# Kernel optimization log

Hardware: AMD Instinct MI355X
Metric: run time of the kernel (lower is better)

The kernel has to match this reference:

```python
import jax, jax.numpy as jnp
import numpy as np

K_CLASSES = 5   # num support classes (5-way)
N_SHOT = 5      # supports per class


def setup_inputs() -> dict:
    key = jax.random.key(0)
    k0, k1, k2, k3 = jax.random.split(key, 4)
    b, bs, c, h, w = 32, K_CLASSES * N_SHOT, 512, 14, 14
    dk, dv = 128, 128
    return {
        "support_features": jax.random.normal(k0, (bs, c, h, w), jnp.float32),
        "query_features": jax.random.normal(k1, (b, c, h, w), jnp.float32),
        "support_labels": jnp.repeat(jnp.arange(K_CLASSES), N_SHOT).astype(jnp.int32),
        "W_qk": jax.random.normal(k2, (dk, c), jnp.float32) * 0.02,  # 1x1 conv weight
        "W_v": jax.random.normal(k3, (dv, c), jnp.float32) * 0.02,   # 1x1 conv weight
    }


def reference(support_features, query_features, support_labels, W_qk, W_v):
    scale = 1.0  # 1/temperature, temperature=1.0
    # 1x1 convs == channel-mixing einsums
    query_q = jnp.einsum('bchw,dc->bdhw', query_features, W_qk)
    query_v = jnp.einsum('bchw,dc->bdhw', query_features, W_v)
    supp_k = jnp.einsum('nchw,dc->ndhw', support_features, W_qk)
    supp_v = jnpveinsum = jnp.einsum('nchw,dc->ndhw', support_features, W_v)
    supp_v = jnpveinsum
    b, cv, h, w = query_v.shape

    # similarity over all supports: [b,h,w,n,i,j] (contracts dim_key)
    sim = jnp.einsum('bchw,ncij->bhwnij', query_q, supp_k) * scale

    # per-class masked softmax over the (n,i,j) axes restricted to that class's
    # supports == index_select + softmax in the original loop (labels balanced).
    cls_mask = support_labels[None, :] == jnp.arange(K_CLASSES)[:, None]  # [K,n]
    neg = jnp.finfo(sim.dtype).min
    sim_k = jnp.where(cls_mask[:, None, None, None, :, None, None], sim[None], neg)  # [K,b,h,w,n,i,j]
    attn = jax.nn.softmax(sim_k.reshape(K_CLASSES, b, h, w, -1), axis=-1)
    attn = attn.reshape(sim_k.shape)  # masked-out entries -> exactly 0

    # weighted sum of support values: [K,b,c,h,w]
    out = jnp.einsum('kbhwnij,ncij->kbchw', attn, supp_v)
    prototypes = jnp.transpose(out, (1, 0, 2, 3, 4)).reshape(b, K_CLASSES, -1)  # b k (c h w)
    query_v_flat = query_v.reshape(b, 1, -1)  # b () (c h w)
    return prototypes, query_v_flat
```

## Files before the change

kernel.cpp:

```cpp
#include <hip/hip_runtime.h>
#include <cstdint>
#include <cstddef>

#define NB   32
#define NSUP 25
#define KCLS 5
#define NC   512
#define ND   128
#define NP   196
#define JS   208
#define NIMG 57
#define SHIFT 8.0f

typedef __attribute__((ext_vector_type(8))) short short8;
typedef __attribute__((ext_vector_type(4))) float floatx4;

__device__ inline short f2bf(float x) {
  union { float f; uint32_t u; } v; v.f = x;
  uint32_t r = (v.u + 0x7FFFu + ((v.u >> 16) & 1u)) >> 16;
  return (short)(r & 0xFFFFu);
}
__device__ inline uint32_t pk2(float a, float b) {
  return (uint32_t)(uint16_t)f2bf(a) | ((uint32_t)(uint16_t)f2bf(b) << 16);
}

__global__ __launch_bounds__(256) void wconv_kernel(
    const float* __restrict__ Wqk, const float* __restrict__ Wv,
    uint16_t* __restrict__ Whi)
{
  const int f = (blockIdx.x * 256 + (int)threadIdx.x) * 8;
  const float* src = (f < ND * NC) ? (Wqk + f) : (Wv + f - ND * NC);
  short8 hv;
  #pragma unroll
  for (int i = 0; i < 8; ++i) hv[i] = f2bf(src[i]);
  *(short8*)(Whi + f) = hv;
}

__global__ __launch_bounds__(256) void gemm_kernel(
    const float* __restrict__ supp, const float* __restrict__ qry,
    const uint16_t* __restrict__ Whi,
    uint16_t* __restrict__ Qt, uint16_t* __restrict__ Kt,
    uint16_t* __restrict__ Vt, float* __restrict__ outVq)
{
  __shared__ float xs[NC * 17];
  const int bx = blockIdx.x;
  const int t16 = bx % 13, img = bx / 13;
  const int tid = (int)threadIdx.x;
  const int w = tid >> 6, lane = tid & 63, ln = lane & 15, q = lane >> 4;
  const int d0 = w * 32;
  const int p0 = t16 * 16;

  const float* __restrict__ X = (img < NB)
      ? (qry  + (size_t)img * NC * NP)
      : (supp + (size_t)(img - NB) * NC * NP);

  for (int idx = tid; idx < NC * 16; idx += 256) {
    const int c = idx >> 4, p = idx & 15;
    int pg = p0 + p; if (pg > NP - 1) pg = NP - 1;
    xs[c * 17 + p] = X[c * NP + pg];
  }
  __syncthreads();

  floatx4 aQ[2], aV[2];
  #pragma unroll
  for (int nt = 0; nt < 2; ++nt) {
    aQ[nt] = (floatx4){0.f, 0.f, 0.f, 0.f};
    aV[nt] = (floatx4){0.f, 0.f, 0.f, 0.f};
  }

  for (int ks = 0; ks < 16; ++ks) {
    short8 xh;
    #pragma unroll
    for (int i = 0; i < 8; ++i)
      xh[i] = f2bf(xs[(ks * 32 + q * 8 + i) * 17 + ln]);
    #pragma unroll
    for (int nt = 0; nt < 2; ++nt) {
      const size_t wr = (size_t)(d0 + nt * 16 + ln) * NC + ks * 32 + q * 8;
      const short8 wqh = *(const short8*)(Whi + wr);
      aQ[nt] = __builtin_amdgcn_mfma_f32_16x16x32_bf16(xh, wqh, aQ[nt], 0, 0, 0);
      const short8 wvh = *(const short8*)(Whi + (size_t)ND * NC + wr);
      aV[nt] = __builtin_amdgcn_mfma_f32_16x16x32_bf16(wvh, xh, aV[nt], 0, 0, 0);
    }
  }

  if (img < NB) {
    #pragma unroll
    for (int nt = 0; nt < 2; ++nt)
      #pragma unroll
      for (int rr = 0; rr < 4; ++rr) {
        const int p = p0 + q * 4 + rr;
        if (p < NP)
          Qt[((size_t)img * NP + p) * ND + d0 + nt * 16 + ln] = (uint16_t)f2bf(aQ[nt][rr]);
      }
  } else {
    const int n = img - NB;
    #pragma unroll
    for (int nt = 0; nt < 2; ++nt)
      #pragma unroll
      for (int rr = 0; rr < 4; ++rr) {
        const int p = p0 + q * 4 + rr;
        Kt[((size_t)n * JS + p) * ND + d0 + nt * 16 + ln] = (uint16_t)f2bf(aQ[nt][rr]);
      }
  }
  const int p = p0 + ln;
  if (img < NB) {
    if (p < NP) {
      #pragma unroll
      for (int nt = 0; nt < 2; ++nt)
        #pragma unroll
        for (int rr = 0; rr < 4; ++rr)
          outVq[((size_t)img * ND + d0 + nt * 16 + q * 4 + rr) * NP + p] = aV[nt][rr];
    }
  } else {
    const int n = img - NB;
    #pragma unroll
    for (int nt = 0; nt < 2; ++nt)
      #pragma unroll
      for (int rr = 0; rr < 4; ++rr)
        Vt[((size_t)n * ND + d0 + nt * 16 + q * 4 + rr) * JS + p] = (uint16_t)f2bf(aV[nt][rr]);
  }
}

__global__ __launch_bounds__(256, 2) void attn_kernel(
    const uint16_t* __restrict__ Qt, const uint16_t* __restrict__ Kt,
    const uint16_t* __restrict__ Vt, const int* __restrict__ labels,
    float* __restrict__ out)
{
  __shared__ float mergeAcc[4][4][256];
  __shared__ float sS[2][4][16];

  const int bx = blockIdx.x;
  const int pt = bx % 13;
  const int rem = bx / 13;
  const int kc = rem % KCLS;
  const int b0 = (rem / KCLS) * 2;
  const int p0 = pt * 16;
  const int tid = (int)threadIdx.x;
  const int w = tid >> 6, lane = tid & 63, ln = lane & 15, q = lane >> 4;

  const int myl = (lane < NSUP) ? labels[lane] : -1;
  unsigned long long m = __ballot(myl == kc);
  int clsPack = 0;
  #pragma unroll
  for (int s = 0; s < 5; ++s) {
    const int n = (m != 0ull) ? (int)__builtin_ctzll(m) : 0;
    clsPack |= n << (6 * s);
    m &= (m - 1);
  }

  short8 aq[2][4];
  #pragma unroll
  for (int bb = 0; bb < 2; ++bb) {
    int p = p0 + ln; if (p > NP - 1) p = NP - 1;
    const uint16_t* base = Qt + ((size_t)(b0 + bb) * NP + p) * ND + q * 8;
    #pragma unroll
    for (int ks = 0; ks < 4; ++ks) aq[bb][ks] = *(const short8*)(base + ks * 32);
  }

  floatx4 acc[2][8];
  #pragma unroll
  for (int bb = 0; bb < 2; ++bb)
    #pragma unroll
    for (int dt = 0; dt < 8; ++dt) acc[bb][dt] = (floatx4){0.f, 0.f, 0.f, 0.f};
  float Ssum[2] = {0.f, 0.f};

  const int alo = (ln + ((q & 1) << 5)) << 2;
  const bool hiTile = (q >= 2);

  for (int it = w; it < 33; it += 4) {
    const int cc = it * 32 + q * 8;
    int s2 = cc / JS, j2 = cc - s2 * JS;
    if (s2 > 4) { s2 = 4; j2 = 192; }
    const int n2 = (clsPack >> (6 * s2)) & 63;
    short8 av[8];
    #pragma unroll
    for (int dt = 0; dt < 8; ++dt)
      av[dt] = *(const short8*)(Vt + ((size_t)n2 * ND + dt * 16 + ln) * JS + j2);

    short8 bk[2][4];
    int jb[2]; bool tval[2];
    #pragma unroll
    for (int t = 0; t < 2; ++t) {
      const int tile16 = it * 2 + t;
      int s = tile16 / 13;
      const int j0 = (tile16 - s * 13) * 16;
      tval[t] = (s < 5); jb[t] = j0;
      if (s > 4) s = 4;
      const int n = (clsPack >> (6 * s)) & 63;
      const uint16_t* kp = Kt + ((size_t)n * JS + j0 + ln) * ND + q * 8;
      #pragma unroll
      for (int ks = 0; ks < 4; ++ks) bk[t][ks] = *(const short8*)(kp + ks * 32);
    }

    #pragma unroll
    for (int bb = 0; bb < 2; ++bb) {
      floatx4 e0, e1;
      #pragma unroll
      for (int t = 0; t < 2; ++t) {
        floatx4 d4 = {0.f, 0.f, 0.f, 0.f};
        #pragma unroll
        for (int ks = 0; ks < 4; ++ks)
          d4 = __builtin_amdgcn_mfma_f32_16x16x32_bf16(bk[t][ks], aq[bb][ks], d4, 0, 0, 0);
        floatx4 ev;
        #pragma unroll
        for (int r = 0; r < 4; ++r) {
          const int j = jb[t] + q * 4 + r;
          const float e = (tval[t] && j < NP) ? __expf(d4[r] - SHIFT) : 0.f;
          ev[r] = e;
          Ssum[bb] += e;
        }
        if (t == 0) e0 = ev; else e1 = ev;
      }

      short8 bp;
      #pragma unroll
      for (int r = 0; r < 4; ++r) {
        const uint32_t pe = pk2(e0[r], e1[r]);
        const int lo = __builtin_amdgcn_ds_bpermute(alo, (int)pe);
        const int hi = __builtin_amdgcn_ds_bpermute(alo + 64, (int)pe);
        bp[r]     = (short)(uint16_t)(hiTile ? (lo >> 16) : (lo & 0xFFFF));
        bp[4 + r] = (short)(uint16_t)(hiTile ? (hi >> 16) : (hi & 0xFFFF));
      }

      #pragma unroll
      for (int dt = 0; dt < 8; ++dt)
        acc[bb][dt] = __builtin_amdgcn_mfma_f32_16x16x32_bf16(av[dt], bp, acc[bb][dt], 0, 0, 0);
    }
  }

  #pragma unroll
  for (int bb = 0; bb < 2; ++bb) {
    float sv = Ssum[bb];
    sv += __shfl_xor(sv, 16);
    sv += __shfl_xor(sv, 32);
    if (lane < 16) sS[bb][w][lane] = sv;
  }
  __syncthreads();
  const float inv0 = 1.f / (sS[0][0][ln] + sS[0][1][ln] + sS[0][2][ln] + sS[0][3][ln]);
  const float inv1 = 1.f / (sS[1][0][ln] + sS[1][1][ln] + sS[1][2][ln] + sS[1][3][ln]);
  const int pp = p0 + ln;

  for (int rd = 0; rd < 4; ++rd) {
    const int bb = rd >> 1, hf = rd & 1;
    #pragma unroll
    for (int g = 0; g < 4; ++g)
      *(floatx4*)&mergeAcc[g][w][lane * 4] = acc[bb][hf * 4 + g];
    __syncthreads();
    floatx4 v = *(const floatx4*)&mergeAcc[w][0][lane * 4];
    v += *(const floatx4*)&mergeAcc[w][1][lane * 4];
    v += *(const floatx4*)&mergeAcc[w][2][lane * 4];
    v += *(const floatx4*)&mergeAcc[w][3][lane * 4];
    if (pp < NP) {
      const float inv = bb ? inv1 : inv0;
      const int dtile = hf * 4 + w;
      float* ob = out + ((size_t)((b0 + bb) * KCLS + kc) * ND + dtile * 16 + q * 4) * NP + pp;
      #pragma unroll
      for (int rr = 0; rr < 4; ++rr) ob[(size_t)rr * NP] = v[rr] * inv;
    }
    __syncthreads();
  }
}

extern "C" void kernel_launch(void* const* d_in, const int* in_sizes, int n_in,
                              void* d_out, int out_size, void* d_ws, size_t ws_size,
                              hipStream_t stream) {
  const float* supp   = (const float*)d_in[0];
  const float* qry    = (const float*)d_in[1];
  const int*   labels = (const int*)d_in[2];
  const float* Wqk    = (const float*)d_in[3];
  const float* Wv     = (const float*)d_in[4];
  float* out = (float*)d_out;

  uint16_t* Whi = (uint16_t*)d_ws;
  uint16_t* Qt  = Whi + (size_t)2 * ND * NC;
  uint16_t* Kt  = Qt  + (size_t)NB * NP * ND;
  uint16_t* Vt  = Kt  + (size_t)NSUP * JS * ND;
  float* outVq = out + (size_t)NB * KCLS * ND * NP;

  wconv_kernel<<<64, 256, 0, stream>>>(Wqk, Wv, Whi);
  gemm_kernel<<<741, 256, 0, stream>>>(supp, qry, Whi, Qt, Kt, Vt, outVq);
  attn_kernel<<<1040, 256, 0, stream>>>(Qt, Kt, Vt, labels, out);
}
```

Measured before the change: 174.1 us.

## Share K/V tiles across batch via double-buffered LDS, bf16-pack gemm inputs in LDS

The attention kernel now has each wave own one query batch (four batches per block) and walk all 33 support chunks. K and V tiles are staged through double-buffered shared memory with register prefetch, so the four waves share one load instead of each wave loading from global memory. This removes the cross-wave accumulator merge and halves the grid, at the cost of a barrier per iteration and more LDS use. The projection GEMM now loads fp32 inputs as vectors, converts them to packed bf16 once into LDS, and reads them back as vector fragments instead of converting eight scalars per step.

```diff
diff --git a/kernel.cpp b/kernel.cpp
--- a/kernel.cpp
+++ b/kernel.cpp
@@ -9,8 +9,14 @@
 #define ND   128
 #define NP   196
 #define JS   208
-#define NIMG 57
 #define SHIFT 8.0f
+
+#define KPITCH 272
+#define KTILE  (16 * KPITCH)
+#define KBUF   (2 * KTILE)
+#define VPITCH 80
+#define VBUF   (128 * VPITCH)
+#define BUFSZ  (KBUF + VBUF)
 
 typedef __attribute__((ext_vector_type(8))) short short8;
 typedef __attribute__((ext_vector_type(4))) float floatx4;
@@ -42,7 +48,7 @@
     uint16_t* __restrict__ Qt, uint16_t* __restrict__ Kt,
     uint16_t* __restrict__ Vt, float* __restrict__ outVq)
 {
-  __shared__ float xs[NC * 17];
+  __shared__ uint16_t xs[16 * 520];
   const int bx = blockIdx.x;
   const int t16 = bx % 13, img = bx / 13;
   const int tid = (int)threadIdx.x;
@@ -54,10 +60,17 @@
       ? (qry  + (size_t)img * NC * NP)
       : (supp + (size_t)(img - NB) * NC * NP);
 
-  for (int idx = tid; idx < NC * 16; idx += 256) {
-    const int c = idx >> 4, p = idx & 15;
-    int pg = p0 + p; if (pg > NP - 1) pg = NP - 1;
-    xs[c * 17 + p] = X[c * NP + pg];
+  #pragma unroll
+  for (int k = 0; k < 4; ++k) {
+    const int id = k * 256 + tid;
+    const int cp = id >> 2;
+    const int pq = id & 3;
+    int pg = p0 + pq * 4; if (pg > NP - 4) pg = NP - 4;
+    const floatx4 fa = *(const floatx4*)(X + (2 * cp) * NP + pg);
+    const floatx4 fb = *(const floatx4*)(X + (2 * cp + 1) * NP + pg);
+    #pragma unroll
+    for (int i = 0; i < 4; ++i)
+      *((uint32_t*)xs + (pq * 4 + i) * 260 + cp) = pk2(fa[i], fb[i]);
   }
   __syncthreads();
 
@@ -69,10 +82,7 @@
   }
 
   for (int ks = 0; ks < 16; ++ks) {
-    short8 xh;
-    #pragma unroll
-    for (int i = 0; i < 8; ++i)
-      xh[i] = f2bf(xs[(ks * 32 + q * 8 + i) * 17 + ln]);
+    const short8 xh = *(const short8*)&xs[ln * 520 + ks * 32 + q * 8];
     #pragma unroll
     for (int nt = 0; nt < 2; ++nt) {
       const size_t wr = (size_t)(d0 + nt * 16 + ln) * NC + ks * 32 + q * 8;
@@ -126,17 +136,17 @@
     const uint16_t* __restrict__ Vt, const int* __restrict__ labels,
     float* __restrict__ out)
 {
-  __shared__ float mergeAcc[4][4][256];
-  __shared__ float sS[2][4][16];
+  __shared__ __align__(16) char smem[2 * BUFSZ];
 
   const int bx = blockIdx.x;
   const int pt = bx % 13;
   const int rem = bx / 13;
   const int kc = rem % KCLS;
-  const int b0 = (rem / KCLS) * 2;
+  const int b0 = (rem / KCLS) * 4;
   const int p0 = pt * 16;
   const int tid = (int)threadIdx.x;
   const int w = tid >> 6, lane = tid & 63, ln = lane & 15, q = lane >> 4;
+  const int b = b0 + w;
 
   const int myl = (lane < NSUP) ? labels[lane] : -1;
   unsigned long long m = __ballot(myl == kc);
@@ -148,116 +158,184 @@
     m &= (m - 1);
   }
 
-  short8 aq[2][4];
-  #pragma unroll
-  for (int bb = 0; bb < 2; ++bb) {
+  short8 aq[4];
+  {
     int p = p0 + ln; if (p > NP - 1) p = NP - 1;
-    const uint16_t* base = Qt + ((size_t)(b0 + bb) * NP + p) * ND + q * 8;
-    #pragma unroll
-    for (int ks = 0; ks < 4; ++ks) aq[bb][ks] = *(const short8*)(base + ks * 32);
-  }
-
-  floatx4 acc[2][8];
-  #pragma unroll
-  for (int bb = 0; bb < 2; ++bb)
-    #pragma unroll
-    for (int dt = 0; dt < 8; ++dt) acc[bb][dt] = (floatx4){0.f, 0.f, 0.f, 0.f};
-  float Ssum[2] = {0.f, 0.f};
+    const uint16_t* base = Qt + ((size_t)b * NP + p) * ND + q * 8;
+    #pragma unroll
+    for (int ks = 0; ks < 4; ++ks) aq[ks] = *(const short8*)(base + ks * 32);
+  }
+
+  floatx4 acc[8];
+  #pragma unroll
+  for (int dt = 0; dt < 8; ++dt) acc[dt] = (floatx4){0.f, 0.f, 0.f, 0.f};
+  float Ssum = 0.f;
 
   const int alo = (ln + ((q & 1) << 5)) << 2;
   const bool hiTile = (q >= 2);
 
-  for (int it = w; it < 33; it += 4) {
-    const int cc = it * 32 + q * 8;
-    int s2 = cc / JS, j2 = cc - s2 * JS;
-    if (s2 > 4) { s2 = 4; j2 = 192; }
-    const int n2 = (clsPack >> (6 * s2)) & 63;
+  int4 pf[4];
+  {
+    int nk[2], j0k[2], nv[2], jv[2];
+    #pragma unroll
+    for (int t = 0; t < 2; ++t) {
+      const int tile16 = t;
+      int s = tile16 / 13;
+      j0k[t] = (tile16 - s * 13) * 16;
+      if (s > 4) s = 4;
+      nk[t] = (clsPack >> (6 * s)) & 63;
+    }
+    #pragma unroll
+    for (int h = 0; h < 2; ++h) {
+      const int ch = h * 16;
+      int sv = ch / JS, jvv = ch - sv * JS;
+      if (sv > 4) { sv = 4; jvv = 192; }
+      nv[h] = (clsPack >> (6 * sv)) & 63;
+      jv[h] = jvv;
+    }
+    #pragma unroll
+    for (int pass = 0; pass < 4; ++pass) {
+      const int slot = pass * 256 + tid;
+      if (pass < 2) {
+        const int t = slot >> 8, r = (slot >> 4) & 15, sc = slot & 15;
+        pf[pass] = *(const int4*)(Kt + ((size_t)(nk[t] * JS + j0k[t] + r)) * ND + sc * 8);
+      } else {
+        const int vs = slot - 512;
+        const int h = vs >> 8, d = (vs >> 1) & 127, sc2 = vs & 1;
+        pf[pass] = *(const int4*)(Vt + ((size_t)(nv[h] * ND + d)) * JS + jv[h] + sc2 * 8);
+      }
+    }
+    char* db = smem;
+    #pragma unroll
+    for (int pass = 0; pass < 4; ++pass) {
+      const int slot = pass * 256 + tid;
+      if (pass < 2) {
+        const int t = slot >> 8, r = (slot >> 4) & 15, sc = slot & 15;
+        *(int4*)(db + t * KTILE + r * KPITCH + sc * 16) = pf[pass];
+      } else {
+        const int vs = slot - 512;
+        const int h = vs >> 8, d = (vs >> 1) & 127, sc2 = vs & 1;
+        *(int4*)(db + KBUF + d * VPITCH + (h * 2 + sc2) * 16) = pf[pass];
+      }
+    }
+  }
+  __syncthreads();
+
+  for (int it = 0; it < 33; ++it) {
+    const int nb = it + 1;
+    int nk[2], j0k[2], nv[2], jv[2];
+    if (nb < 33) {
+      #pragma unroll
+      for (int t = 0; t < 2; ++t) {
+        const int tile16 = nb * 2 + t;
+        int s = tile16 / 13;
+        j0k[t] = (tile16 - s * 13) * 16;
+        if (s > 4) s = 4;
+        nk[t] = (clsPack >> (6 * s)) & 63;
+      }
+      #pragma unroll
+      for (int h = 0; h < 2; ++h) {
+        const int ch = nb * 32 + h * 16;
+        int sv = ch / JS, jvv = ch - sv * JS;
+        if (sv > 4) { sv = 4; jvv = 192; }
+        nv[h] = (clsPack >> (6 * sv)) & 63;
+        jv[h] = jvv;
+      }
+      #pragma unroll
+      for (int pass = 0; pass < 4; ++pass) {
+        const int slot = pass * 256 + tid;
+        if (pass < 2) {
+          const int t = slot >> 8, r = (slot >> 4) & 15, sc = slot & 15;
+          pf[pass] = *(const int4*)(Kt + ((size_t)(nk[t] * JS + j0k[t] + r)) * ND + sc * 8);
+        } else {
+          const int vs = slot - 512;
+          const int h = vs >> 8, d = (vs >> 1) & 127, sc2 = vs & 1;
+          pf[pass] = *(const int4*)(Vt + ((size_t)(nv[h] * ND + d)) * JS + jv[h] + sc2 * 8);
+        }
+      }
+    }
+
+    const char* kb = smem + (it & 1) * BUFSZ;
+    const char* vb = kb + KBUF;
+
     short8 av[8];
     #pragma unroll
     for (int dt = 0; dt < 8; ++dt)
-      av[dt] = *(const short8*)(Vt + ((size_t)n2 * ND + dt * 16 + ln) * JS + j2);
+      av[dt] = *(const short8*)(vb + (dt * 16 + ln) * VPITCH + q * 16);
 
     short8 bk[2][4];
-    int jb[2]; bool tval[2];
+    #pragma unroll
+    for (int t = 0; t < 2; ++t)
+      #pragma unroll
+      for (int ks = 0; ks < 4; ++ks)
+        bk[t][ks] = *(const short8*)(kb + t * KTILE + ln * KPITCH + ks * 64 + q * 16);
+
+    floatx4 e0, e1;
     #pragma unroll
     for (int t = 0; t < 2; ++t) {
       const int tile16 = it * 2 + t;
-      int s = tile16 / 13;
+      const int s = tile16 / 13;
       const int j0 = (tile16 - s * 13) * 16;
-      tval[t] = (s < 5); jb[t] = j0;
-      if (s > 4) s = 4;
-      const int n = (clsPack >> (6 * s)) & 63;
-      const uint16_t* kp = Kt + ((size_t)n * JS + j0 + ln) * ND + q * 8;
-      #pragma unroll
-      for (int ks = 0; ks < 4; ++ks) bk[t][ks] = *(const short8*)(kp + ks * 32);
-    }
-
-    #pragma unroll
-    for (int bb = 0; bb < 2; ++bb) {
-      floatx4 e0, e1;
-      #pragma unroll
-      for (int t = 0; t < 2; ++t) {
-        floatx4 d4 = {0.f, 0.f, 0.f, 0.f};
-        #pragma unroll
-        for (int ks = 0; ks < 4; ++ks)
-          d4 = __builtin_amdgcn_mfma_f32_16x16x32_bf16(bk[t][ks], aq[bb][ks], d4, 0, 0, 0);
-        floatx4 ev;
-        #pragma unroll
-        for (int r = 0; r < 4; ++r) {
-          const int j = jb[t] + q * 4 + r;
-          const float e = (tval[t] && j < NP) ? __expf(d4[r] - SHIFT) : 0.f;
-          ev[r] = e;
-          Ssum[bb] += e;
+      const bool tval = (s < 5);
+      floatx4 d4 = {0.f, 0.f, 0.f, 0.f};
+      #pragma unroll
+      for (int ks = 0; ks < 4; ++ks)
+        d4 = __builtin_amdgcn_mfma_f32_16x16x32_bf16(bk[t][ks], aq[ks], d4, 0, 0, 0);
+      floatx4 ev;
+      #pragma unroll
+      for (int r = 0; r < 4; ++r) {
+        const int j = j0 + q * 4 + r;
+        const float e = (tval && j < NP) ? __expf(d4[r] - SHIFT) : 0.f;
+        ev[r] = e;
+        Ssum += e;
+      }
+      if (t == 0) e0 = ev; else e1 = ev;
+    }
+
+    short8 bp;
+    #pragma unroll
+    for (int r = 0; r < 4; ++r) {
+      const uint32_t pe = pk2(e0[r], e1[r]);
+      const int lo = __builtin_amdgcn_ds_bpermute(alo, (int)pe);
+      const int hi = __builtin_amdgcn_ds_bpermute(alo + 64, (int)pe);
+      bp[r]     = (short)(uint16_t)(hiTile ? (lo >> 16) : (lo & 0xFFFF));
+      bp[4 + r] = (short)(uint16_t)(hiTile ? (hi >> 16) : (hi & 0xFFFF));
+    }
+
+    #pragma unroll
+    for (int dt = 0; dt < 8; ++dt)
+      acc[dt] = __builtin_amdgcn_mfma_f32_16x16x32_bf16(av[dt], bp, acc[dt], 0, 0, 0);
+
+    if (nb < 33) {
+      char* db = smem + (nb & 1) * BUFSZ;
+      #pragma unroll
+      for (int pass = 0; pass < 4; ++pass) {
+        const int slot = pass * 256 + tid;
+        if (pass < 2) {
+          const int t = slot >> 8, r = (slot >> 4) & 15, sc = slot & 15;
+          *(int4*)(db + t * KTILE + r * KPITCH + sc * 16) = pf[pass];
+        } else {
+          const int vs = slot - 512;
+          const int h = vs >> 8, d = (vs >> 1) & 127, sc2 = vs & 1;
+          *(int4*)(db + KBUF + d * VPITCH + (h * 2 + sc2) * 16) = pf[pass];
         }
-        if (t == 0) e0 = ev; else e1 = ev;
-      }
-
-      short8 bp;
-      #pragma unroll
-      for (int r = 0; r < 4; ++r) {
-        const uint32_t pe = pk2(e0[r], e1[r]);
-        const int lo = __builtin_amdgcn_ds_bpermute(alo, (int)pe);
-        const int hi = __builtin_amdgcn_ds_bpermute(alo + 64, (int)pe);
-        bp[r]     = (short)(uint16_t)(hiTile ? (lo >> 16) : (lo & 0xFFFF));
-        bp[4 + r] = (short)(uint16_t)(hiTile ? (hi >> 16) : (hi & 0xFFFF));
-      }
-
-      #pragma unroll
-      for (int dt = 0; dt < 8; ++dt)
-        acc[bb][dt] = __builtin_amdgcn_mfma_f32_16x16x32_bf16(av[dt], bp, acc[bb][dt], 0, 0, 0);
-    }
-  }
-
-  #pragma unroll
-  for (int bb = 0; bb < 2; ++bb) {
-    float sv = Ssum[bb];
-    sv += __shfl_xor(sv, 16);
-    sv += __shfl_xor(sv, 32);
-    if (lane < 16) sS[bb][w][lane] = sv;
-  }
-  __syncthreads();
-  const float inv0 = 1.f / (sS[0][0][ln] + sS[0][1][ln] + sS[0][2][ln] + sS[0][3][ln]);
-  const float inv1 = 1.f / (sS[1][0][ln] + sS[1][1][ln] + sS[1][2][ln] + sS[1][3][ln]);
+      }
+    }
+    __syncthreads();
+  }
+
+  float sv = Ssum;
+  sv += __shfl_xor(sv, 16);
+  sv += __shfl_xor(sv, 32);
+  const float inv = 1.f / sv;
   const int pp = p0 + ln;
-
-  for (int rd = 0; rd < 4; ++rd) {
-    const int bb = rd >> 1, hf = rd & 1;
-    #pragma unroll
-    for (int g = 0; g < 4; ++g)
-      *(floatx4*)&mergeAcc[g][w][lane * 4] = acc[bb][hf * 4 + g];
-    __syncthreads();
-    floatx4 v = *(const floatx4*)&mergeAcc[w][0][lane * 4];
-    v += *(const floatx4*)&mergeAcc[w][1][lane * 4];
-    v += *(const floatx4*)&mergeAcc[w][2][lane * 4];
-    v += *(const floatx4*)&mergeAcc[w][3][lane * 4];
-    if (pp < NP) {
-      const float inv = bb ? inv1 : inv0;
-      const int dtile = hf * 4 + w;
-      float* ob = out + ((size_t)((b0 + bb) * KCLS + kc) * ND + dtile * 16 + q * 4) * NP + pp;
-      #pragma unroll
-      for (int rr = 0; rr < 4; ++rr) ob[(size_t)rr * NP] = v[rr] * inv;
-    }
-    __syncthreads();
+  if (pp < NP) {
+    float* ob = out + ((size_t)(b * KCLS + kc) * ND + q * 4) * NP + pp;
+    #pragma unroll
+    for (int dt = 0; dt < 8; ++dt)
+      #pragma unroll
+      for (int rr = 0; rr < 4; ++rr)
+        ob[(size_t)(dt * 16 + rr) * NP] = acc[dt][rr] * inv;
   }
 }
 
@@ -279,5 +357,5 @@
 
   wconv_kernel<<<64, 256, 0, stream>>>(Wqk, Wv, Whi);
   gemm_kernel<<<741, 256, 0, stream>>>(supp, qry, Whi, Qt, Kt, Vt, outVq);
-  attn_kernel<<<1040, 256, 0, stream>>>(Qt, Kt, Vt, labels, out);
-}
+  attn_kernel<<<520, 256, 0, stream>>>(Qt, Kt, Vt, labels, out);
+}
```

Measured after the change: 161.1 us. -7.5%, faster.
